# Kernel tuning notes

Measured on AMD Instinct MI355X. Metric: run time of the kernel, lower is better.

## Reference

```python
import jax, jax.numpy as jnp
import numpy as np

N_NODES = 50000
N_EDGES = 800000
D_IN = 96
D_OUT = 96


def setup_inputs() -> dict:
    key = jax.random.key(0)
    k1, k2, k3, k4, k5, k6 = jax.random.split(key, 6)
    x = jax.random.normal(k1, (N_NODES, D_IN), dtype=jnp.float32)
    edge_index = jax.random.randint(k2, (2, N_EDGES), 0, N_NODES, dtype=jnp.int32)
    W_lin = jax.random.normal(k3, (D_OUT, D_IN), dtype=jnp.float32) * 0.1
    b_lin = jax.random.normal(k4, (D_OUT,), dtype=jnp.float32) * 0.1
    W_root = jax.random.normal(k5, (D_OUT, D_IN), dtype=jnp.float32) * 0.1
    b_root = jax.random.normal(k6, (D_OUT,), dtype=jnp.float32) * 0.1
    return {"x": x, "edge_index": edge_index, "W_lin": W_lin, "b_lin": b_lin,
            "W_root": W_root, "b_root": b_root}


def reference(x, edge_index, W_lin, b_lin, W_root, b_root):
    # GCNConv with separate root weight: out = relu(scatter_add(norm * lin(x_src), dst) + root(x))
    src, dst = edge_index[0], edge_index[1]
    n = x.shape[0]
    # symmetric degree normalization (in-degree based, clamped to avoid div0)
    deg = jax.ops.segment_sum(jnp.ones(src.shape[0], dtype=x.dtype), dst, num_segments=n)
    dinv = jax.lax.rsqrt(jnp.maximum(deg, 1.0))
    norm = dinv[src] * dinv[dst]                      # [E]
    h = x @ W_lin.T + b_lin                           # [N, D_OUT] neighbor transform
    msgs = h[src] * norm[:, None]                     # [E, D_OUT] gathered + scaled
    agg = jax.ops.segment_sum(msgs, dst, num_segments=n)  # scatter-add
    out = agg + x @ W_root.T + b_root                 # root/self contribution
    return jax.nn.relu(out)
```

## Files before the change

### kernel.cpp

```cpp
#include <hip/hip_runtime.h>

#define D 96
#define BSH 5
#define SCAP 1088
#define SBSH 8
#define NSBMAX 224
#define SBCAP 4608
#define CH 2048

typedef __attribute__((ext_vector_type(8))) short bf16x8;
typedef __attribute__((ext_vector_type(4))) float f32x4;

__device__ __forceinline__ unsigned bf16_rne(float f) {
    unsigned u = __float_as_uint(f);
    return (u + 0x7fffu + ((u >> 16) & 1u)) >> 16;
}
__device__ __forceinline__ float blo(unsigned u) { return __uint_as_float(u << 16); }
__device__ __forceinline__ float bhi(unsigned u) { return __uint_as_float(u & 0xffff0000u); }

__global__ __launch_bounds__(512) void prep_kernel(
    const int* __restrict__ ei, int* __restrict__ scur, unsigned* __restrict__ sp,
    int* __restrict__ deg, const float* __restrict__ Wlin,
    const float* __restrict__ Wroot, unsigned* __restrict__ wfrag,
    const float* __restrict__ x, unsigned* __restrict__ xs,
    int E, int NSB, int n)
{
    __shared__ int hist[NSBMAX];
    __shared__ int lstart[NSBMAX];
    __shared__ int gbase[NSBMAX];
    __shared__ unsigned stage[CH];
    int t = threadIdx.x;
    int gt = blockIdx.x * 512 + t;
    int e0 = blockIdx.x * CH;
    int ne = min(CH, E - e0);
    for (int i = t; i < NSB; i += 512) hist[i] = 0;
    if (gt < 9216) {
        int f = gt >> 8, r = gt & 255;
        int l = r >> 2, jp = r & 3;
        int ct = f / 6, st = f % 6;
        int nn = ct * 16 + (l & 15);
        int k  = st * 32 + (l >> 4) * 8 + jp * 2;
        const float* W = (k < D) ? Wlin : Wroot;
        int kk = (k < D) ? k : k - D;
        float v0 = W[nn * D + kk], v1 = W[nn * D + kk + 1];
        wfrag[gt] = bf16_rne(v0) | (bf16_rne(v1) << 16);
    }
    __syncthreads();
    unsigned pk[4]; int bk[4];
    int base = e0 + t * 4;
    if (base + 3 < E) {
        int4 a = *(const int4*)(ei + base);
        int4 b = *(const int4*)(ei + E + base);
        pk[0] = (unsigned)a.x | ((unsigned)b.x << 16); bk[0] = b.x >> SBSH;
        pk[1] = (unsigned)a.y | ((unsigned)b.y << 16); bk[1] = b.y >> SBSH;
        pk[2] = (unsigned)a.z | ((unsigned)b.z << 16); bk[2] = b.z >> SBSH;
        pk[3] = (unsigned)a.w | ((unsigned)b.w << 16); bk[3] = b.w >> SBSH;
        atomicAdd(&deg[b.x], 1);
        atomicAdd(&deg[b.y], 1);
        atomicAdd(&deg[b.z], 1);
        atomicAdd(&deg[b.w], 1);
    } else {
        #pragma unroll
        for (int u = 0; u < 4; ++u) {
            int e = base + u;
            if (e < E) {
                int dd = ei[E + e];
                pk[u] = (unsigned)ei[e] | ((unsigned)dd << 16); bk[u] = dd >> SBSH;
                atomicAdd(&deg[dd], 1);
            } else bk[u] = -1;
        }
    }
    #pragma unroll
    for (int u = 0; u < 4; ++u)
        if (bk[u] >= 0) atomicAdd(&hist[bk[u]], 1);
    __syncthreads();
    if (t < 64) {
        int carry = 0;
        for (int c0 = 0; c0 < NSB; c0 += 64) {
            int i = c0 + t;
            int v = (i < NSB) ? hist[i] : 0;
            int incl = v;
            #pragma unroll
            for (int d = 1; d < 64; d <<= 1) {
                int uu = __shfl_up(incl, d, 64);
                if (t >= d) incl += uu;
            }
            if (i < NSB) lstart[i] = carry + incl - v;
            carry += __shfl(incl, 63, 64);
        }
    }
    __syncthreads();
    for (int i = t; i < NSB; i += 512) {
        int c = hist[i];
        if (c > 0) gbase[i] = atomicAdd(&scur[i], c);
        hist[i] = lstart[i];
    }
    __syncthreads();
    #pragma unroll
    for (int u = 0; u < 4; ++u) {
        if (bk[u] >= 0) {
            int p = atomicAdd(&hist[bk[u]], 1);
            stage[p] = pk[u];
        }
    }
    __syncthreads();
    for (int i = t; i < ne; i += 512) {
        unsigned w = stage[i];
        int sb = (int)(w >> (16 + SBSH));
        int slot = gbase[sb] + (i - lstart[sb]);
        if (slot < SBCAP) sp[(size_t)sb * SBCAP + slot] = w;
    }
    int gsz = gridDim.x * 512;
    int ntask = (n + 1) * 24;
    for (int i = gt; i < ntask; i += gsz) {
        int row = i / 24, q = i - row * 24;
        uint2 o;
        if (row < n) {
            float4 v = ((const float4*)x)[(size_t)row * 24 + q];
            o.x = bf16_rne(v.x) | (bf16_rne(v.y) << 16);
            o.y = bf16_rne(v.z) | (bf16_rne(v.w) << 16);
        } else { o.x = 0u; o.y = 0u; }
        *(uint2*)(xs + (size_t)row * 48 + q * 2) = o;
    }
}

__global__ __launch_bounds__(256, 7) void bgather_gemm_kernel(
    const int* __restrict__ scur, const unsigned* __restrict__ sp,
    const int* __restrict__ deg, const unsigned* __restrict__ xs,
    const unsigned* __restrict__ wfrag, const float* __restrict__ blin,
    const float* __restrict__ broot, float* __restrict__ out, int n)
{
    __shared__ uint2 sd[SCAP];
    __shared__ int histC[32];
    __shared__ int seg[33];
    __shared__ int cur[32];
    __shared__ int pq;
    __shared__ unsigned yt[32][52];
    __shared__ float sv32[32];
    int t = threadIdx.x;
    int nwg = gridDim.x;
    int qq = nwg >> 3, rr = nwg & 7;
    int xcd = blockIdx.x & 7, ix = blockIdx.x >> 3;
    int bid = (xcd < rr ? xcd * (qq + 1) : rr * (qq + 1) + (xcd - rr) * qq) + ix;
    int node0 = bid << BSH;
    int sb = bid >> 3;
    int lb = bid & 7;
    int ne = min(scur[sb], SBCAP);
    const unsigned* spb = sp + (size_t)sb * SBCAP;
    const unsigned ZR = (unsigned)n;
    if (t < 32) {
        int node = node0 + t;
        histC[t] = (node < n) ? deg[node] : 0;
    }
    if (t >= 32 && t < 40) sd[t - 32] = make_uint2(ZR, 0u);
    __syncthreads();
    if (t == 0) {
        int run = 8;
        #pragma unroll
        for (int i = 0; i < 32; ++i) {
            seg[i] = run;
            run += (histC[i] + 7) & ~7;
            if (run > SCAP) run = SCAP;
        }
        seg[32] = run;
        pq = 0;
    }
    __syncthreads();
    if (t < 32) cur[t] = seg[t];
    __syncthreads();
    for (int i0 = t * 4; i0 < ne; i0 += 1024) {
        if (i0 + 3 < ne) {
            uint4 w4 = *(const uint4*)(spb + i0);
            if (((w4.x >> (16 + BSH)) & 7) == (unsigned)lb) { int p = atomicAdd(&cur[(w4.x >> 16) & 31], 1); if (p < SCAP) sd[p].x = w4.x & 0xffffu; }
            if (((w4.y >> (16 + BSH)) & 7) == (unsigned)lb) { int p = atomicAdd(&cur[(w4.y >> 16) & 31], 1); if (p < SCAP) sd[p].x = w4.y & 0xffffu; }
            if (((w4.z >> (16 + BSH)) & 7) == (unsigned)lb) { int p = atomicAdd(&cur[(w4.z >> 16) & 31], 1); if (p < SCAP) sd[p].x = w4.z & 0xffffu; }
            if (((w4.w >> (16 + BSH)) & 7) == (unsigned)lb) { int p = atomicAdd(&cur[(w4.w >> 16) & 31], 1); if (p < SCAP) sd[p].x = w4.w & 0xffffu; }
        } else {
            for (int i = i0; i < ne; ++i) {
                unsigned w = spb[i];
                if (((w >> (16 + BSH)) & 7) == (unsigned)lb) { int p = atomicAdd(&cur[(w >> 16) & 31], 1); if (p < SCAP) sd[p].x = w & 0xffffu; }
            }
        }
    }
    __syncthreads();
    if (t < 32) {
        int e = seg[t + 1];
        int s = seg[t] + histC[t]; if (s > e) s = e;
        for (int p2 = s; p2 < e; ++p2) sd[p2] = make_uint2(ZR, 0u);
    }
    __syncthreads();
    int tot = seg[32];
    for (int i = t; i < tot; i += 256) {
        unsigned idx = sd[i].x;
        float y = 0.f;
        if (idx != ZR) {
            int d = deg[idx];
            y = rsqrtf((float)(d > 1 ? d : 1));
        }
        sd[i].y = __float_as_uint(y);
    }
    __syncthreads();

    int l = t & 63;
    int g = l / 12;
    int m = l - g * 12;
    unsigned loff = (unsigned)(m << 4);
    const char* xb = (const char*)xs;

    for (;;) {
        int p;
        if (l == 0) p = atomicAdd(&pq, 1);
        p = __builtin_amdgcn_readfirstlane(p);
        if (p >= 16) break;
        int ndA = p * 2, ndB = ndA + 1;
        int jsA = seg[ndA], itA = (seg[ndA + 1] - jsA) >> 3;
        int jsB = seg[ndB], itB = (seg[ndB + 1] - jsB) >> 3;
        int iters = itA > itB ? itA : itB;
        float aA0=0.f,aA1=0.f,aA2=0.f,aA3=0.f,aA4=0.f,aA5=0.f,aA6=0.f,aA7=0.f;
        float aB0=0.f,aB1=0.f,aB2=0.f,aB3=0.f,aB4=0.f,aB5=0.f,aB6=0.f,aB7=0.f;
        float sn = 0.f;
        for (int it = 0; it < iters; ++it) {
            int baseA = (it < itA) ? (jsA + it * 8) : 0;
            int baseB = (it < itB) ? (jsB + it * 8) : 0;
            if (l < 48) {
                uint2 qA0 = sd[baseA + g], qA1 = sd[baseA + 4 + g];
                uint2 qB0 = sd[baseB + g], qB1 = sd[baseB + 4 + g];
                uint4 vA0 = *(const uint4*)(xb + qA0.x * 192u + loff);
                uint4 vA1 = *(const uint4*)(xb + qA1.x * 192u + loff);
                uint4 vB0 = *(const uint4*)(xb + qB0.x * 192u + loff);
                uint4 vB1 = *(const uint4*)(xb + qB1.x * 192u + loff);
                float dA0 = __uint_as_float(qA0.y), dA1 = __uint_as_float(qA1.y);
                float dB0 = __uint_as_float(qB0.y), dB1 = __uint_as_float(qB1.y);
                aA0 += dA0 * blo(vA0.x); aA1 += dA0 * bhi(vA0.x); aA2 += dA0 * blo(vA0.y); aA3 += dA0 * bhi(vA0.y);
                aA4 += dA0 * blo(vA0.z); aA5 += dA0 * bhi(vA0.z); aA6 += dA0 * blo(vA0.w); aA7 += dA0 * bhi(vA0.w);
                aA0 += dA1 * blo(vA1.x); aA1 += dA1 * bhi(vA1.x); aA2 += dA1 * blo(vA1.y); aA3 += dA1 * bhi(vA1.y);
                aA4 += dA1 * blo(vA1.z); aA5 += dA1 * bhi(vA1.z); aA6 += dA1 * blo(vA1.w); aA7 += dA1 * bhi(vA1.w);
                aB0 += dB0 * blo(vB0.x); aB1 += dB0 * bhi(vB0.x); aB2 += dB0 * blo(vB0.y); aB3 += dB0 * bhi(vB0.y);
                aB4 += dB0 * blo(vB0.z); aB5 += dB0 * bhi(vB0.z); aB6 += dB0 * blo(vB0.w); aB7 += dB0 * bhi(vB0.w);
                aB0 += dB1 * blo(vB1.x); aB1 += dB1 * bhi(vB1.x); aB2 += dB1 * blo(vB1.y); aB3 += dB1 * bhi(vB1.y);
                aB4 += dB1 * blo(vB1.z); aB5 += dB1 * bhi(vB1.z); aB6 += dB1 * blo(vB1.w); aB7 += dB1 * bhi(vB1.w);
            } else {
                int bs = (l < 56) ? baseA : baseB;
                sn += __uint_as_float(sd[bs + (l & 7)].y);
            }
        }
        float stA = 0.f, stB = 0.f;
        #pragma unroll
        for (int u = 0; u < 8; ++u) {
            stA += __shfl(sn, 48 + u, 64);
            stB += __shfl(sn, 56 + u, 64);
        }
        int l24 = (l + 24) & 63, l12 = (l + 12) & 63;
        aA0 += __shfl(aA0, l24, 64); aA1 += __shfl(aA1, l24, 64); aA2 += __shfl(aA2, l24, 64); aA3 += __shfl(aA3, l24, 64);
        aA4 += __shfl(aA4, l24, 64); aA5 += __shfl(aA5, l24, 64); aA6 += __shfl(aA6, l24, 64); aA7 += __shfl(aA7, l24, 64);
        aB0 += __shfl(aB0, l24, 64); aB1 += __shfl(aB1, l24, 64); aB2 += __shfl(aB2, l24, 64); aB3 += __shfl(aB3, l24, 64);
        aB4 += __shfl(aB4, l24, 64); aB5 += __shfl(aB5, l24, 64); aB6 += __shfl(aB6, l24, 64); aB7 += __shfl(aB7, l24, 64);
        aA0 += __shfl(aA0, l12, 64); aA1 += __shfl(aA1, l12, 64); aA2 += __shfl(aA2, l12, 64); aA3 += __shfl(aA3, l12, 64);
        aA4 += __shfl(aA4, l12, 64); aA5 += __shfl(aA5, l12, 64); aA6 += __shfl(aA6, l12, 64); aA7 += __shfl(aA7, l12, 64);
        aB0 += __shfl(aB0, l12, 64); aB1 += __shfl(aB1, l12, 64); aB2 += __shfl(aB2, l12, 64); aB3 += __shfl(aB3, l12, 64);
        aB4 += __shfl(aB4, l12, 64); aB5 += __shfl(aB5, l12, 64); aB6 += __shfl(aB6, l12, 64); aB7 += __shfl(aB7, l12, 64);
        int nodeA = node0 + ndA, nodeB = node0 + ndB;
        float dnA = (nodeA < n) ? rsqrtf((float)(histC[ndA] > 1 ? histC[ndA] : 1)) : 0.f;
        float dnB = (nodeB < n) ? rsqrtf((float)(histC[ndB] > 1 ? histC[ndB] : 1)) : 0.f;
        if (l < 12) {
            uint4 oA, oB;
            oA.x = bf16_rne(dnA * aA0) | (bf16_rne(dnA * aA1) << 16);
            oA.y = bf16_rne(dnA * aA2) | (bf16_rne(dnA * aA3) << 16);
            oA.z = bf16_rne(dnA * aA4) | (bf16_rne(dnA * aA5) << 16);
            oA.w = bf16_rne(dnA * aA6) | (bf16_rne(dnA * aA7) << 16);
            oB.x = bf16_rne(dnB * aB0) | (bf16_rne(dnB * aB1) << 16);
            oB.y = bf16_rne(dnB * aB2) | (bf16_rne(dnB * aB3) << 16);
            oB.z = bf16_rne(dnB * aB4) | (bf16_rne(dnB * aB5) << 16);
            oB.w = bf16_rne(dnB * aB6) | (bf16_rne(dnB * aB7) << 16);
            *(uint4*)&yt[ndA][4 * m] = oA;
            *(uint4*)&yt[ndB][4 * m] = oB;
        } else if (l == 48) {
            sv32[ndA] = dnA * stA;
            sv32[ndB] = dnB * stB;
        }
    }
    __syncthreads();

    int wv = t >> 6;
    int lane15 = l & 15, quad = l >> 4;
    for (int j = wv; j < 12; j += 4) {
        int rg = j / 6, ct = j % 6;
        int r0 = node0 + rg * 16;
        f32x4 accY = (f32x4){0.f, 0.f, 0.f, 0.f};
        f32x4 accX = (f32x4){0.f, 0.f, 0.f, 0.f};
        #pragma unroll
        for (int st_ = 0; st_ < 3; ++st_) {
            bf16x8 a = *(const bf16x8*)(&yt[rg * 16 + lane15][st_ * 16 + quad * 4]);
            bf16x8 b = *(const bf16x8*)(wfrag + ((ct * 6 + st_) * 64 + l) * 4);
            accY = __builtin_amdgcn_mfma_f32_16x16x32_bf16(a, b, accY, 0, 0, 0);
        }
        int ar = r0 + lane15;
        #pragma unroll
        for (int sm = 0; sm < 3; ++sm) {
            bf16x8 a = (bf16x8){0, 0, 0, 0, 0, 0, 0, 0};
            if (ar < n) a = *(const bf16x8*)(xs + (size_t)ar * 48 + sm * 16 + quad * 4);
            bf16x8 b = *(const bf16x8*)(wfrag + ((ct * 6 + 3 + sm) * 64 + l) * 4);
            accX = __builtin_amdgcn_mfma_f32_16x16x32_bf16(a, b, accX, 0, 0, 0);
        }
        int col = ct * 16 + lane15;
        float blc = blin[col], brc = broot[col];
        #pragma unroll
        for (int reg = 0; reg < 4; ++reg) {
            int r = r0 + quad * 4 + reg;
            if (r < n) {
                float sv = sv32[rg * 16 + quad * 4 + reg];
                float v = accY[reg] + accX[reg] + sv * blc + brc;
                out[(size_t)r * D + col] = fmaxf(v, 0.f);
            }
        }
    }
}

extern "C" void kernel_launch(void* const* d_in, const int* in_sizes, int n_in,
                              void* d_out, int out_size, void* d_ws, size_t ws_size,
                              hipStream_t stream) {
    const float* x     = (const float*)d_in[0];
    const int*   ei    = (const int*)d_in[1];
    const float* Wlin  = (const float*)d_in[2];
    const float* blin  = (const float*)d_in[3];
    const float* Wroot = (const float*)d_in[4];
    const float* broot = (const float*)d_in[5];
    float* out = (float*)d_out;

    const int n = in_sizes[0] / D;
    const int E = in_sizes[1] / 2;
    const int NB = (n + 31) >> BSH;
    const int NSB = (n + 255) >> SBSH;
    const int NBLK = (E + CH - 1) / CH;

    int*      scur  = (int*)d_ws;
    int*      deg   = (int*)(scur + 256);
    unsigned* sp    = (unsigned*)(deg + n + 4);
    unsigned* wfrag = sp + (size_t)NSB * SBCAP;
    unsigned* xs    = wfrag + 9216;

    hipMemsetAsync(scur, 0, (256 + n + 4) * sizeof(int), stream);

    prep_kernel<<<NBLK, 512, 0, stream>>>(ei, scur, sp, deg, Wlin, Wroot,
                                          wfrag, x, xs, E, NSB, n);
    bgather_gemm_kernel<<<NB, 256, 0, stream>>>(scur, sp, deg, xs, wfrag,
                                                blin, broot, out, n);
}
```

Before: 164.4 us.

## Software-pipeline neighbor gathers and move degree atomics after edge staging

The gather loop in the fused gather+GEMM kernel now loads the next iteration's edge descriptors and bf16 feature rows while it accumulates the current ones, to hide global-load latency. Occupancy hint drops from 7 to 4 waves per SIMD so the doubled live registers fit. In the prep kernel, per-edge degree atomics move later, after staging, and global bucket bases are kept in registers until a later barrier. The cost is higher register pressure and lower occupancy, which may reduce latency hiding from other waves.

New measurement: 178.7 us. 1.09x slower.

```diff
diff --git a/kernel.cpp b/kernel.cpp
--- a/kernel.cpp
+++ b/kernel.cpp
@@ -33,7 +33,7 @@
     int gt = blockIdx.x * 512 + t;
     int e0 = blockIdx.x * CH;
     int ne = min(CH, E - e0);
-    for (int i = t; i < NSB; i += 512) hist[i] = 0;
+    if (t < NSB) hist[t] = 0;
     if (gt < 9216) {
         int f = gt >> 8, r = gt & 255;
         int l = r >> 2, jp = r & 3;
@@ -55,19 +55,12 @@
         pk[1] = (unsigned)a.y | ((unsigned)b.y << 16); bk[1] = b.y >> SBSH;
         pk[2] = (unsigned)a.z | ((unsigned)b.z << 16); bk[2] = b.z >> SBSH;
         pk[3] = (unsigned)a.w | ((unsigned)b.w << 16); bk[3] = b.w >> SBSH;
-        atomicAdd(&deg[b.x], 1);
-        atomicAdd(&deg[b.y], 1);
-        atomicAdd(&deg[b.z], 1);
-        atomicAdd(&deg[b.w], 1);
     } else {
         #pragma unroll
         for (int u = 0; u < 4; ++u) {
             int e = base + u;
-            if (e < E) {
-                int dd = ei[E + e];
-                pk[u] = (unsigned)ei[e] | ((unsigned)dd << 16); bk[u] = dd >> SBSH;
-                atomicAdd(&deg[dd], 1);
-            } else bk[u] = -1;
+            if (e < E) { pk[u] = (unsigned)ei[e] | ((unsigned)ei[E + e] << 16); bk[u] = ei[E + e] >> SBSH; }
+            else bk[u] = -1;
         }
     }
     #pragma unroll
@@ -90,10 +83,11 @@
         }
     }
     __syncthreads();
-    for (int i = t; i < NSB; i += 512) {
-        int c = hist[i];
-        if (c > 0) gbase[i] = atomicAdd(&scur[i], c);
-        hist[i] = lstart[i];
+    int myBase = 0;
+    if (t < NSB) {
+        int c = hist[t];
+        if (c > 0) myBase = atomicAdd(&scur[t], c);
+        hist[t] = lstart[t];
     }
     __syncthreads();
     #pragma unroll
@@ -104,6 +98,11 @@
         }
     }
     __syncthreads();
+    if (t < NSB) gbase[t] = myBase;
+    __syncthreads();
+    #pragma unroll
+    for (int u = 0; u < 4; ++u)
+        if (bk[u] >= 0) atomicAdd(&deg[pk[u] >> 16], 1);
     for (int i = t; i < ne; i += 512) {
         unsigned w = stage[i];
         int sb = (int)(w >> (16 + SBSH));
@@ -124,7 +123,7 @@
     }
 }
 
-__global__ __launch_bounds__(256, 7) void bgather_gemm_kernel(
+__global__ __launch_bounds__(256, 4) void bgather_gemm_kernel(
     const int* __restrict__ scur, const unsigned* __restrict__ sp,
     const int* __restrict__ deg, const unsigned* __restrict__ xs,
     const unsigned* __restrict__ wfrag, const float* __restrict__ blin,
@@ -219,16 +218,46 @@
         float aA0=0.f,aA1=0.f,aA2=0.f,aA3=0.f,aA4=0.f,aA5=0.f,aA6=0.f,aA7=0.f;
         float aB0=0.f,aB1=0.f,aB2=0.f,aB3=0.f,aB4=0.f,aB5=0.f,aB6=0.f,aB7=0.f;
         float sn = 0.f;
+        uint2 qA0, qA1, qB0, qB1;
+        uint4 vA0, vA1, vB0, vB1;
+        float sv = 0.f;
+        if (iters > 0) {
+            int baseA = (itA > 0) ? jsA : 0;
+            int baseB = (itB > 0) ? jsB : 0;
+            if (l < 48) {
+                qA0 = sd[baseA + g]; qA1 = sd[baseA + 4 + g];
+                qB0 = sd[baseB + g]; qB1 = sd[baseB + 4 + g];
+                vA0 = *(const uint4*)(xb + qA0.x * 192u + loff);
+                vA1 = *(const uint4*)(xb + qA1.x * 192u + loff);
+                vB0 = *(const uint4*)(xb + qB0.x * 192u + loff);
+                vB1 = *(const uint4*)(xb + qB1.x * 192u + loff);
+            } else {
+                int bs = (l < 56) ? baseA : baseB;
+                sv = __uint_as_float(sd[bs + (l & 7)].y);
+            }
+        }
         for (int it = 0; it < iters; ++it) {
-            int baseA = (it < itA) ? (jsA + it * 8) : 0;
-            int baseB = (it < itB) ? (jsB + it * 8) : 0;
+            int nxt = it + 1;
+            bool pf = nxt < iters;
+            uint2 nqA0, nqA1, nqB0, nqB1;
+            uint4 nvA0, nvA1, nvB0, nvB1;
+            float nsv = 0.f;
+            if (pf) {
+                int baseA2 = (nxt < itA) ? (jsA + nxt * 8) : 0;
+                int baseB2 = (nxt < itB) ? (jsB + nxt * 8) : 0;
+                if (l < 48) {
+                    nqA0 = sd[baseA2 + g]; nqA1 = sd[baseA2 + 4 + g];
+                    nqB0 = sd[baseB2 + g]; nqB1 = sd[baseB2 + 4 + g];
+                    nvA0 = *(const uint4*)(xb + nqA0.x * 192u + loff);
+                    nvA1 = *(const uint4*)(xb + nqA1.x * 192u + loff);
+                    nvB0 = *(const uint4*)(xb + nqB0.x * 192u + loff);
+                    nvB1 = *(const uint4*)(xb + nqB1.x * 192u + loff);
+                } else {
+                    int bs2 = (l < 56) ? baseA2 : baseB2;
+                    nsv = __uint_as_float(sd[bs2 + (l & 7)].y);
+                }
+            }
             if (l < 48) {
-                uint2 qA0 = sd[baseA + g], qA1 = sd[baseA + 4 + g];
-                uint2 qB0 = sd[baseB + g], qB1 = sd[baseB + 4 + g];
-                uint4 vA0 = *(const uint4*)(xb + qA0.x * 192u + loff);
-                uint4 vA1 = *(const uint4*)(xb + qA1.x * 192u + loff);
-                uint4 vB0 = *(const uint4*)(xb + qB0.x * 192u + loff);
-                uint4 vB1 = *(const uint4*)(xb + qB1.x * 192u + loff);
                 float dA0 = __uint_as_float(qA0.y), dA1 = __uint_as_float(qA1.y);
                 float dB0 = __uint_as_float(qB0.y), dB1 = __uint_as_float(qB1.y);
                 aA0 += dA0 * blo(vA0.x); aA1 += dA0 * bhi(vA0.x); aA2 += dA0 * blo(vA0.y); aA3 += dA0 * bhi(vA0.y);
@@ -240,8 +269,12 @@
                 aB0 += dB1 * blo(vB1.x); aB1 += dB1 * bhi(vB1.x); aB2 += dB1 * blo(vB1.y); aB3 += dB1 * bhi(vB1.y);
                 aB4 += dB1 * blo(vB1.z); aB5 += dB1 * bhi(vB1.z); aB6 += dB1 * blo(vB1.w); aB7 += dB1 * bhi(vB1.w);
             } else {
-                int bs = (l < 56) ? baseA : baseB;
-                sn += __uint_as_float(sd[bs + (l & 7)].y);
+                sn += sv;
+            }
+            if (pf) {
+                qA0 = nqA0; qA1 = nqA1; qB0 = nqB0; qB1 = nqB1;
+                vA0 = nvA0; vA1 = nvA1; vB0 = nvB0; vB1 = nvB1;
+                sv = nsv;
             }
         }
         float stA = 0.f, stB = 0.f;
@@ -308,8 +341,8 @@
         for (int reg = 0; reg < 4; ++reg) {
             int r = r0 + quad * 4 + reg;
             if (r < n) {
-                float sv = sv32[rg * 16 + quad * 4 + reg];
-                float v = accY[reg] + accX[reg] + sv * blc + brc;
+                float sv2 = sv32[rg * 16 + quad * 4 + reg];
+                float v = accY[reg] + accX[reg] + sv2 * blc + brc;
                 out[(size_t)r * D + col] = fmaxf(v, 0.f);
             }
         }
```

## Replace global degree atomics with per-bucket shared histograms and split prep blocks

Applied to the files above, without the earlier changes.

Removes the per-edge global atomicAdd on deg. In-degree is now computed by dedicated blocks, each scanning a quarter of the dst array for one 256-node bucket, building a shared-memory histogram and flushing it with one global atomic per node. The x-to-bf16 conversion moves to its own set of 256 blocks so it is no longer serialized after edge binning. The gather kernel recomputes its local node degrees from the bucketed edge list instead of reading deg, and its occupancy hint rises from 7 to 8. This trades global atomic contention for redundant dst scans (about 196×4 blocks each read a slice of dst) and an extra pass over the edge list in the gather kernel.

Measured after the change: 177.3 us. +7.8%, slower.

```diff
diff --git a/kernel.cpp b/kernel.cpp
--- a/kernel.cpp
+++ b/kernel.cpp
@@ -7,6 +7,8 @@
 #define NSBMAX 224
 #define SBCAP 4608
 #define CH 2048
+#define XB 256
+#define DSL 4
 
 typedef __attribute__((ext_vector_type(8))) short bf16x8;
 typedef __attribute__((ext_vector_type(4))) float f32x4;
@@ -23,115 +25,146 @@
     int* __restrict__ deg, const float* __restrict__ Wlin,
     const float* __restrict__ Wroot, unsigned* __restrict__ wfrag,
     const float* __restrict__ x, unsigned* __restrict__ xs,
-    int E, int NSB, int n)
+    int E, int NSB, int n, int NBLK)
 {
     __shared__ int hist[NSBMAX];
     __shared__ int lstart[NSBMAX];
     __shared__ int gbase[NSBMAX];
     __shared__ unsigned stage[CH];
     int t = threadIdx.x;
-    int gt = blockIdx.x * 512 + t;
-    int e0 = blockIdx.x * CH;
-    int ne = min(CH, E - e0);
-    for (int i = t; i < NSB; i += 512) hist[i] = 0;
-    if (gt < 9216) {
-        int f = gt >> 8, r = gt & 255;
-        int l = r >> 2, jp = r & 3;
-        int ct = f / 6, st = f % 6;
-        int nn = ct * 16 + (l & 15);
-        int k  = st * 32 + (l >> 4) * 8 + jp * 2;
-        const float* W = (k < D) ? Wlin : Wroot;
-        int kk = (k < D) ? k : k - D;
-        float v0 = W[nn * D + kk], v1 = W[nn * D + kk + 1];
-        wfrag[gt] = bf16_rne(v0) | (bf16_rne(v1) << 16);
-    }
-    __syncthreads();
-    unsigned pk[4]; int bk[4];
-    int base = e0 + t * 4;
-    if (base + 3 < E) {
-        int4 a = *(const int4*)(ei + base);
-        int4 b = *(const int4*)(ei + E + base);
-        pk[0] = (unsigned)a.x | ((unsigned)b.x << 16); bk[0] = b.x >> SBSH;
-        pk[1] = (unsigned)a.y | ((unsigned)b.y << 16); bk[1] = b.y >> SBSH;
-        pk[2] = (unsigned)a.z | ((unsigned)b.z << 16); bk[2] = b.z >> SBSH;
-        pk[3] = (unsigned)a.w | ((unsigned)b.w << 16); bk[3] = b.w >> SBSH;
-        atomicAdd(&deg[b.x], 1);
-        atomicAdd(&deg[b.y], 1);
-        atomicAdd(&deg[b.z], 1);
-        atomicAdd(&deg[b.w], 1);
+    int blk = blockIdx.x;
+
+    if (blk < NBLK) {
+        int gt = blk * 512 + t;
+        int e0 = blk * CH;
+        int ne = min(CH, E - e0);
+        if (t < NSB) hist[t] = 0;
+        if (gt < 9216) {
+            int f = gt >> 8, r = gt & 255;
+            int l = r >> 2, jp = r & 3;
+            int ct = f / 6, st = f % 6;
+            int nn = ct * 16 + (l & 15);
+            int k  = st * 32 + (l >> 4) * 8 + jp * 2;
+            const float* W = (k < D) ? Wlin : Wroot;
+            int kk = (k < D) ? k : k - D;
+            float v0 = W[nn * D + kk], v1 = W[nn * D + kk + 1];
+            wfrag[gt] = bf16_rne(v0) | (bf16_rne(v1) << 16);
+        }
+        __syncthreads();
+        unsigned pk[4]; int bk[4];
+        int base = e0 + t * 4;
+        if (base + 3 < E) {
+            int4 a = *(const int4*)(ei + base);
+            int4 b = *(const int4*)(ei + E + base);
+            pk[0] = (unsigned)a.x | ((unsigned)b.x << 16); bk[0] = b.x >> SBSH;
+            pk[1] = (unsigned)a.y | ((unsigned)b.y << 16); bk[1] = b.y >> SBSH;
+            pk[2] = (unsigned)a.z | ((unsigned)b.z << 16); bk[2] = b.z >> SBSH;
+            pk[3] = (unsigned)a.w | ((unsigned)b.w << 16); bk[3] = b.w >> SBSH;
+        } else {
+            #pragma unroll
+            for (int u = 0; u < 4; ++u) {
+                int e = base + u;
+                if (e < E) { pk[u] = (unsigned)ei[e] | ((unsigned)ei[E + e] << 16); bk[u] = ei[E + e] >> SBSH; }
+                else bk[u] = -1;
+            }
+        }
+        #pragma unroll
+        for (int u = 0; u < 4; ++u)
+            if (bk[u] >= 0) atomicAdd(&hist[bk[u]], 1);
+        __syncthreads();
+        if (t < 64) {
+            int carry = 0;
+            for (int c0 = 0; c0 < NSB; c0 += 64) {
+                int i = c0 + t;
+                int v = (i < NSB) ? hist[i] : 0;
+                int incl = v;
+                #pragma unroll
+                for (int d = 1; d < 64; d <<= 1) {
+                    int uu = __shfl_up(incl, d, 64);
+                    if (t >= d) incl += uu;
+                }
+                if (i < NSB) lstart[i] = carry + incl - v;
+                carry += __shfl(incl, 63, 64);
+            }
+        }
+        __syncthreads();
+        for (int i = t; i < NSB; i += 512) {
+            int c = hist[i];
+            if (c > 0) gbase[i] = atomicAdd(&scur[i], c);
+            hist[i] = lstart[i];
+        }
+        __syncthreads();
+        #pragma unroll
+        for (int u = 0; u < 4; ++u) {
+            if (bk[u] >= 0) {
+                int p = atomicAdd(&hist[bk[u]], 1);
+                stage[p] = pk[u];
+            }
+        }
+        __syncthreads();
+        for (int i = t; i < ne; i += 512) {
+            unsigned w = stage[i];
+            int sb = (int)(w >> (16 + SBSH));
+            int slot = gbase[sb] + (i - lstart[sb]);
+            if (slot < SBCAP) sp[(size_t)sb * SBCAP + slot] = w;
+        }
+    } else if (blk < NBLK + XB) {
+        int pb = blk - NBLK;
+        int gt = pb * 512 + t;
+        int gsz = XB * 512;
+        int ntask = (n + 1) * 24;
+        for (int i = gt; i < ntask; i += gsz) {
+            int row = i / 24, q = i - row * 24;
+            uint2 o;
+            if (row < n) {
+                float4 v = ((const float4*)x)[(size_t)row * 24 + q];
+                o.x = bf16_rne(v.x) | (bf16_rne(v.y) << 16);
+                o.y = bf16_rne(v.z) | (bf16_rne(v.w) << 16);
+            } else { o.x = 0u; o.y = 0u; }
+            *(uint2*)(xs + (size_t)row * 48 + q * 2) = o;
+        }
     } else {
-        #pragma unroll
-        for (int u = 0; u < 4; ++u) {
-            int e = base + u;
-            if (e < E) {
-                int dd = ei[E + e];
-                pk[u] = (unsigned)ei[e] | ((unsigned)dd << 16); bk[u] = dd >> SBSH;
-                atomicAdd(&deg[dd], 1);
-            } else bk[u] = -1;
-        }
-    }
-    #pragma unroll
-    for (int u = 0; u < 4; ++u)
-        if (bk[u] >= 0) atomicAdd(&hist[bk[u]], 1);
-    __syncthreads();
-    if (t < 64) {
-        int carry = 0;
-        for (int c0 = 0; c0 < NSB; c0 += 64) {
-            int i = c0 + t;
-            int v = (i < NSB) ? hist[i] : 0;
-            int incl = v;
-            #pragma unroll
-            for (int d = 1; d < 64; d <<= 1) {
-                int uu = __shfl_up(incl, d, 64);
-                if (t >= d) incl += uu;
-            }
-            if (i < NSB) lstart[i] = carry + incl - v;
-            carry += __shfl(incl, 63, 64);
-        }
-    }
-    __syncthreads();
-    for (int i = t; i < NSB; i += 512) {
-        int c = hist[i];
-        if (c > 0) gbase[i] = atomicAdd(&scur[i], c);
-        hist[i] = lstart[i];
-    }
-    __syncthreads();
-    #pragma unroll
-    for (int u = 0; u < 4; ++u) {
-        if (bk[u] >= 0) {
-            int p = atomicAdd(&hist[bk[u]], 1);
-            stage[p] = pk[u];
-        }
-    }
-    __syncthreads();
-    for (int i = t; i < ne; i += 512) {
-        unsigned w = stage[i];
-        int sb = (int)(w >> (16 + SBSH));
-        int slot = gbase[sb] + (i - lstart[sb]);
-        if (slot < SBCAP) sp[(size_t)sb * SBCAP + slot] = w;
-    }
-    int gsz = gridDim.x * 512;
-    int ntask = (n + 1) * 24;
-    for (int i = gt; i < ntask; i += gsz) {
-        int row = i / 24, q = i - row * 24;
-        uint2 o;
-        if (row < n) {
-            float4 v = ((const float4*)x)[(size_t)row * 24 + q];
-            o.x = bf16_rne(v.x) | (bf16_rne(v.y) << 16);
-            o.y = bf16_rne(v.z) | (bf16_rne(v.w) << 16);
-        } else { o.x = 0u; o.y = 0u; }
-        *(uint2*)(xs + (size_t)row * 48 + q * 2) = o;
+        int db = blk - NBLK - XB;
+        int w  = db >> 2;
+        int s  = db & (DSL - 1);
+        int* h = (int*)stage;
+        if (t < 256) h[t] = 0;
+        __syncthreads();
+        int qsz = (E + DSL - 1) / DSL;
+        int lo = s * qsz;
+        int hi = min(E, lo + qsz);
+        const int* dst = ei + E;
+        for (int i0 = lo + t * 4; i0 < hi; i0 += 2048) {
+            if (i0 + 3 < hi) {
+                int4 d4 = *(const int4*)(dst + i0);
+                if ((d4.x >> SBSH) == w) atomicAdd(&h[d4.x & 255], 1);
+                if ((d4.y >> SBSH) == w) atomicAdd(&h[d4.y & 255], 1);
+                if ((d4.z >> SBSH) == w) atomicAdd(&h[d4.z & 255], 1);
+                if ((d4.w >> SBSH) == w) atomicAdd(&h[d4.w & 255], 1);
+            } else {
+                for (int i = i0; i < hi; ++i) {
+                    int dd = dst[i];
+                    if ((dd >> SBSH) == w) atomicAdd(&h[dd & 255], 1);
+                }
+            }
+        }
+        __syncthreads();
+        if (t < 256) {
+            int c = h[t];
+            int node = (w << SBSH) + t;
+            if (c > 0 && node < n) atomicAdd(&deg[node], c);
+        }
     }
 }
 
-__global__ __launch_bounds__(256, 7) void bgather_gemm_kernel(
+__global__ __launch_bounds__(256, 8) void bgather_gemm_kernel(
     const int* __restrict__ scur, const unsigned* __restrict__ sp,
     const int* __restrict__ deg, const unsigned* __restrict__ xs,
     const unsigned* __restrict__ wfrag, const float* __restrict__ blin,
     const float* __restrict__ broot, float* __restrict__ out, int n)
 {
     __shared__ uint2 sd[SCAP];
-    __shared__ int histC[32];
+    __shared__ int hist[32];
     __shared__ int seg[33];
     __shared__ int cur[32];
     __shared__ int pq;
@@ -148,18 +181,30 @@
     int ne = min(scur[sb], SBCAP);
     const unsigned* spb = sp + (size_t)sb * SBCAP;
     const unsigned ZR = (unsigned)n;
-    if (t < 32) {
-        int node = node0 + t;
-        histC[t] = (node < n) ? deg[node] : 0;
-    }
-    if (t >= 32 && t < 40) sd[t - 32] = make_uint2(ZR, 0u);
+    if (t < 32) hist[t] = 0;
+    if (t < 8) sd[t] = make_uint2(ZR, 0u);
+    __syncthreads();
+    for (int i0 = t * 4; i0 < ne; i0 += 1024) {
+        if (i0 + 3 < ne) {
+            uint4 w4 = *(const uint4*)(spb + i0);
+            if (((w4.x >> (16 + BSH)) & 7) == (unsigned)lb) atomicAdd(&hist[(w4.x >> 16) & 31], 1);
+            if (((w4.y >> (16 + BSH)) & 7) == (unsigned)lb) atomicAdd(&hist[(w4.y >> 16) & 31], 1);
+            if (((w4.z >> (16 + BSH)) & 7) == (unsigned)lb) atomicAdd(&hist[(w4.z >> 16) & 31], 1);
+            if (((w4.w >> (16 + BSH)) & 7) == (unsigned)lb) atomicAdd(&hist[(w4.w >> 16) & 31], 1);
+        } else {
+            for (int i = i0; i < ne; ++i) {
+                unsigned w = spb[i];
+                if (((w >> (16 + BSH)) & 7) == (unsigned)lb) atomicAdd(&hist[(w >> 16) & 31], 1);
+            }
+        }
+    }
     __syncthreads();
     if (t == 0) {
         int run = 8;
         #pragma unroll
         for (int i = 0; i < 32; ++i) {
             seg[i] = run;
-            run += (histC[i] + 7) & ~7;
+            run += (hist[i] + 7) & ~7;
             if (run > SCAP) run = SCAP;
         }
         seg[32] = run;
@@ -185,7 +230,7 @@
     __syncthreads();
     if (t < 32) {
         int e = seg[t + 1];
-        int s = seg[t] + histC[t]; if (s > e) s = e;
+        int s = seg[t] + hist[t]; if (s > e) s = e;
         for (int p2 = s; p2 < e; ++p2) sd[p2] = make_uint2(ZR, 0u);
     }
     __syncthreads();
@@ -260,8 +305,8 @@
         aB0 += __shfl(aB0, l12, 64); aB1 += __shfl(aB1, l12, 64); aB2 += __shfl(aB2, l12, 64); aB3 += __shfl(aB3, l12, 64);
         aB4 += __shfl(aB4, l12, 64); aB5 += __shfl(aB5, l12, 64); aB6 += __shfl(aB6, l12, 64); aB7 += __shfl(aB7, l12, 64);
         int nodeA = node0 + ndA, nodeB = node0 + ndB;
-        float dnA = (nodeA < n) ? rsqrtf((float)(histC[ndA] > 1 ? histC[ndA] : 1)) : 0.f;
-        float dnB = (nodeB < n) ? rsqrtf((float)(histC[ndB] > 1 ? histC[ndB] : 1)) : 0.f;
+        float dnA = (nodeA < n) ? rsqrtf((float)(hist[ndA] > 1 ? hist[ndA] : 1)) : 0.f;
+        float dnB = (nodeB < n) ? rsqrtf((float)(hist[ndB] > 1 ? hist[ndB] : 1)) : 0.f;
         if (l < 12) {
             uint4 oA, oB;
             oA.x = bf16_rne(dnA * aA0) | (bf16_rne(dnA * aA1) << 16);
@@ -341,8 +386,9 @@
 
     hipMemsetAsync(scur, 0, (256 + n + 4) * sizeof(int), stream);
 
-    prep_kernel<<<NBLK, 512, 0, stream>>>(ei, scur, sp, deg, Wlin, Wroot,
-                                          wfrag, x, xs, E, NSB, n);
+    int pgrid = NBLK + XB + NSB * DSL;
+    prep_kernel<<<pgrid, 512, 0, stream>>>(ei, scur, sp, deg, Wlin, Wroot,
+                                           wfrag, x, xs, E, NSB, n, NBLK);
     bgather_gemm_kernel<<<NB, 256, 0, stream>>>(scur, sp, deg, xs, wfrag,
                                                 blin, broot, out, n);
 }
```
